# Kernel optimization log

Hardware: AMD Instinct MI355X
Metric: run time of the kernel (lower is better)

## Reference

```python
import jax, jax.numpy as jnp
import numpy as np

B, D, C, Q = 4096, 128, 1000, 65536
PROTO_M = 0.99
EPS = 1e-12


def _l2norm(x, axis=-1):
    n = jnp.sqrt(jnp.sum(x * x, axis=axis, keepdims=True))
    return x / jnp.maximum(n, EPS)


def setup_inputs() -> dict:
    key = jax.random.key(0)
    ks = jax.random.split(key, 7)
    q = _l2norm(jax.random.normal(ks[0], (B, D), dtype=jnp.float32))
    k = _l2norm(jax.random.normal(ks[1], (B, D), dtype=jnp.float32))
    classfy_logits = jax.random.normal(ks[2], (B, C), dtype=jnp.float32)
    plabel = jax.random.uniform(ks[3], (B, C), dtype=jnp.float32)
    prototypes = _l2norm(jax.random.normal(ks[4], (C, D), dtype=jnp.float32))
    queue = _l2norm(jax.random.normal(ks[5], (Q, D), dtype=jnp.float32))
    queue_pseudo = jax.random.randint(ks[6], (Q,), 0, C).astype(jnp.float32)
    return {
        "q": q, "k": k, "classfy_logits": classfy_logits, "plabel": plabel,
        "prototypes": prototypes, "queue": queue, "queue_pseudo": queue_pseudo,
        "ptr": 0,
    }


def reference(q, k, classfy_logits, plabel, prototypes, queue, queue_pseudo, ptr):
    m = PROTO_M
    # classifier softmax (encoder head output)
    classfy_out = jax.nn.softmax(classfy_logits, axis=1)          # [B, C]
    # cluster logits against OLD prototypes (mm happens before EMA update)
    logits_prot = jnp.matmul(q, prototypes.T)                     # [B, C]
    cluster_out = jax.nn.softmax(logits_prot, axis=1)
    # pseudo labels from partial-label-masked scores
    pseudo_labels = jnp.argmax(classfy_out * plabel, axis=1)      # [B] int
    # --- vectorized order-dependent scatter-EMA prototype update ---
    # sequential: proto[l_i] = m*proto[l_i] + (1-m)*q_i  for i = 0..B-1
    # closed form: proto[c]*m^{n_c} + sum_i (1-m)*m^{(#later samples with same label)} q_i
    onehot = (pseudo_labels[:, None] == jnp.arange(C)[None, :])   # [B, C] bool
    counts = jnp.sum(onehot, axis=0)                              # [C] n_c
    rank = jnp.take_along_axis(jnp.cumsum(onehot.astype(jnp.int32), axis=0),
                               pseudo_labels[:, None], axis=1)[:, 0] - 1  # [B]
    n_l = counts[pseudo_labels]                                   # [B]
    w = (1.0 - m) * jnp.power(jnp.float32(m), (n_l - 1 - rank).astype(jnp.float32))
    scatter = jnp.zeros_like(prototypes).at[pseudo_labels].add(w[:, None] * q)
    decay = jnp.power(jnp.float32(m), counts.astype(jnp.float32))[:, None]
    new_prototypes = _l2norm(prototypes * decay + scatter, axis=1)
    # --- MoCo queue enqueue/dequeue (contrastive bank uses OLD queue) ---
    cont_features = jnp.concatenate([q, k, queue], axis=0)        # [2B+Q, D]
    pl_f = pseudo_labels.astype(jnp.float32)
    cont_labels = jnp.concatenate([pl_f, pl_f, queue_pseudo], axis=0)
    new_queue = jax.lax.dynamic_update_slice(queue, k, (ptr, 0))
    new_queue_pseudo = jax.lax.dynamic_update_slice(queue_pseudo, pl_f, (ptr,))
    new_ptr = (ptr + q.shape[0]) % queue.shape[0]
    return (classfy_out, cluster_out, cont_features, cont_labels,
            new_prototypes, new_queue, new_queue_pseudo, new_ptr)
```

## Files before the change

### kernel.cpp

```cpp
#include <hip/hip_runtime.h>
#include <hip/hip_bf16.h>
#include <math.h>

#define Bn 4096
#define Dn 128
#define Cn 1000
#define Qn 65536
#define CPAD 1024

typedef __attribute__((ext_vector_type(8))) short short8v;
typedef __attribute__((ext_vector_type(4))) short short4v;
typedef __attribute__((ext_vector_type(4))) float f32x4;
typedef __attribute__((ext_vector_type(4))) float f4v;

__device__ inline float waveAllMaxF(float v) {
    for (int o = 32; o; o >>= 1) v = fmaxf(v, __shfl_xor(v, o));
    return v;
}
__device__ inline float waveAllSumF(float v) {
    for (int o = 32; o; o >>= 1) v += __shfl_xor(v, o);
    return v;
}
__device__ inline float waveSumF(float v) {
    for (int o = 32; o; o >>= 1) v += __shfl_down(v, o);
    return v;
}
__device__ inline short f2bf(float x) {
    union { __hip_bfloat16 h; short s; } u;
    u.h = __float2bfloat16(x);
    return u.s;
}

__global__ __launch_bounds__(256) void k_phase1(
    const float* __restrict__ logits, const float* __restrict__ plabel,
    const float* __restrict__ q, const float* __restrict__ proto,
    const float* __restrict__ kk, const float* __restrict__ queue,
    const int* __restrict__ ptrp,
    float* __restrict__ out_cls, int* __restrict__ labels,
    __hip_bfloat16* __restrict__ qb, __hip_bfloat16* __restrict__ pb,
    float* __restrict__ out_feat, float* __restrict__ out_queue)
{
    int bid = blockIdx.x, t = threadIdx.x;
    int g = bid / 3, s = bid % 3;

    if (s != 0) {
        int cidx = g * 2 + (s - 1);
        int p = *ptrp;
        int pc = p < 0 ? 0 : (p > Qn - Bn ? Qn - Bn : p);
        const long long QD = (long long)Bn * Dn;
        const long long n4 = (2 * QD + (long long)Qn * Dn) / 4;
        const long long stride = 2048LL * 256;
        for (long long i = (long long)cidx * 256 + t; i < n4; i += stride) {
            long long off = i * 4;
            if (off < QD) {
                *(f4v*)(out_feat + off) = *(const f4v*)(q + off);
            } else if (off < 2 * QD) {
                *(f4v*)(out_feat + off) = *(const f4v*)(kk + off - QD);
            } else {
                long long qoff = off - 2 * QD;
                f4v v = *(const f4v*)(queue + qoff);
                *(f4v*)(out_feat + off) = v;
                int row = (int)(qoff >> 7);
                int col = (int)(qoff & 127);
                unsigned rr = (unsigned)(row - pc);
                if (rr < (unsigned)Bn) v = *(const f4v*)(kk + (long long)rr * Dn + col);
                *(f4v*)(out_queue + qoff) = v;
            }
        }
        return;
    }

    if (t < 160) {
        int idx4 = g * 160 + t;
        if (idx4 < 131072) {
            f4v v = *(const f4v*)(q + (long long)idx4 * 4);
            short4v o = {f2bf(v.x), f2bf(v.y), f2bf(v.z), f2bf(v.w)};
            *(short4v*)((short*)qb + (long long)idx4 * 4) = o;
        } else {
            int j4 = idx4 - 131072;
            short4v o = {0, 0, 0, 0};
            if (j4 < 32000) {
                f4v v = *(const f4v*)(proto + (long long)j4 * 4);
                o = (short4v){f2bf(v.x), f2bf(v.y), f2bf(v.z), f2bf(v.w)};
            }
            *(short4v*)((short*)pb + (long long)j4 * 4) = o;
        }
    }

    int lane = t & 63, wid = t >> 6;
    int row = g * 4 + wid;
    const float* x = logits + (long long)row * Cn;

    float vv[16];
    float mx = -INFINITY;
#pragma unroll
    for (int j = 0; j < 4; ++j) {
        int f4i = lane + j * 64;
        f4v v = (f4v){-INFINITY, -INFINITY, -INFINITY, -INFINITY};
        if (f4i < 250) v = *(const f4v*)(x + f4i * 4);
        vv[j * 4 + 0] = v.x; vv[j * 4 + 1] = v.y;
        vv[j * 4 + 2] = v.z; vv[j * 4 + 3] = v.w;
        mx = fmaxf(mx, fmaxf(fmaxf(v.x, v.y), fmaxf(v.z, v.w)));
    }
    mx = waveAllMaxF(mx);

    float ssum = 0.f;
#pragma unroll
    for (int u = 0; u < 16; ++u) {
        vv[u] = expf(vv[u] - mx);
        ssum += vv[u];
    }
    ssum = waveAllSumF(ssum);
    float inv = 1.f / ssum;

    float bv = -INFINITY; int bi = Cn;
#pragma unroll
    for (int j = 0; j < 4; ++j) {
        int f4i = lane + j * 64;
        if (f4i < 250) {
            float o0 = vv[j * 4 + 0] * inv, o1 = vv[j * 4 + 1] * inv;
            float o2 = vv[j * 4 + 2] * inv, o3 = vv[j * 4 + 3] * inv;
            *((f4v*)(out_cls + (long long)row * Cn) + f4i) = (f4v){o0, o1, o2, o3};
            f4v p4 = *((const f4v*)(plabel + (long long)row * Cn) + f4i);
            float pr[4] = {o0 * p4.x, o1 * p4.y, o2 * p4.z, o3 * p4.w};
#pragma unroll
            for (int jj = 0; jj < 4; ++jj) {
                if (pr[jj] > bv) { bv = pr[jj]; bi = f4i * 4 + jj; }
            }
        }
    }
    for (int o = 32; o; o >>= 1) {
        float ov = __shfl_xor(bv, o);
        int   oi = __shfl_xor(bi, o);
        if (ov > bv || (ov == bv && oi < bi)) { bv = ov; bi = oi; }
    }
    if (lane == 0) labels[row] = bi;
}

__global__ __launch_bounds__(256) void k_phase2(
    const __hip_bfloat16* __restrict__ qb, const __hip_bfloat16* __restrict__ pb,
    const float* __restrict__ proto, const float* __restrict__ q,
    const int* __restrict__ lbl, const float* __restrict__ qps,
    const int* __restrict__ ptrp,
    float* __restrict__ outC, float* __restrict__ outp,
    float* __restrict__ out_lab, float* __restrict__ out_qps,
    float* __restrict__ out_ptr)
{
    __shared__ __align__(16) char smem[32800];
    int bid = blockIdx.x, t = threadIdx.x;

    if (bid < 256) {
        float (*red)[4] = (float (*)[4])smem;
        int lane = t & 63, w = t >> 6;
        int la = lane & 15, lk = lane >> 4;
        int row0 = bid * 16;

        f32x4 acc[16];
#pragma unroll
        for (int j = 0; j < 16; ++j) acc[j] = (f32x4){0.f, 0.f, 0.f, 0.f};

        const short* A = (const short*)qb + (long long)(row0 + la) * Dn;
        const short* Bp = (const short*)pb;
#pragma unroll
        for (int kc = 0; kc < Dn; kc += 32) {
            short8v a = *(const short8v*)(A + kc + lk * 8);
#pragma unroll
            for (int j = 0; j < 16; ++j) {
                int prow = w * 256 + j * 16 + la;
                short8v b = *(const short8v*)(Bp + (long long)prow * Dn + kc + lk * 8);
                acc[j] = __builtin_amdgcn_mfma_f32_16x16x32_bf16(a, b, acc[j], 0, 0, 0);
            }
        }

        float m[4];
#pragma unroll
        for (int rg = 0; rg < 4; ++rg) {
            float v = -INFINITY;
#pragma unroll
            for (int j = 0; j < 16; ++j) {
                int col = w * 256 + j * 16 + la;
                if (col < Cn) v = fmaxf(v, acc[j][rg]);
            }
#pragma unroll
            for (int o = 1; o < 16; o <<= 1) v = fmaxf(v, __shfl_xor(v, o));
            m[rg] = v;
        }
        if (la == 0) {
#pragma unroll
            for (int rg = 0; rg < 4; ++rg) red[lk * 4 + rg][w] = m[rg];
        }
        __syncthreads();
#pragma unroll
        for (int rg = 0; rg < 4; ++rg) {
            int r = lk * 4 + rg;
            m[rg] = fmaxf(fmaxf(red[r][0], red[r][1]), fmaxf(red[r][2], red[r][3]));
        }
        __syncthreads();

        float s[4];
#pragma unroll
        for (int rg = 0; rg < 4; ++rg) {
            float v = 0.f;
#pragma unroll
            for (int j = 0; j < 16; ++j) {
                int col = w * 256 + j * 16 + la;
                float e = (col < Cn) ? expf(acc[j][rg] - m[rg]) : 0.f;
                acc[j][rg] = e;
                v += e;
            }
#pragma unroll
            for (int o = 1; o < 16; o <<= 1) v += __shfl_xor(v, o);
            s[rg] = v;
        }
        if (la == 0) {
#pragma unroll
            for (int rg = 0; rg < 4; ++rg) red[lk * 4 + rg][w] = s[rg];
        }
        __syncthreads();
#pragma unroll
        for (int rg = 0; rg < 4; ++rg) {
            int r = lk * 4 + rg;
            s[rg] = 1.f / (red[r][0] + red[r][1] + red[r][2] + red[r][3]);
        }

#pragma unroll
        for (int j = 0; j < 16; ++j) {
            int col = w * 256 + j * 16 + la;
            if (col < Cn) {
                int rowb = row0 + lk * 4;
#pragma unroll
                for (int rg = 0; rg < 4; ++rg)
                    outC[(long long)(rowb + rg) * Cn + col] = acc[j][rg] * s[rg];
            }
        }
    } else if (bid < 756) {
        int* sl = (int*)smem;
        unsigned short* list0 = (unsigned short*)(smem + 16384);
        unsigned short* list1 = list0 + 4096;
        int* nm = (int*)(smem + 32768);
        float* shh = (float*)(smem + 32776);

        int h = t >> 7, tt = t & 127;
        int c = (bid - 256) * 2 + h;

#pragma unroll
        for (int u = 0; u < 4; ++u) {
            int base = (u * 256 + t) * 4;
            *(int4*)(sl + base) = *(const int4*)(lbl + base);
        }
        if (t == 0)   nm[0] = 0;
        if (t == 128) nm[1] = 0;
        __syncthreads();

        int wv = t >> 6;
        if ((wv & 1) == 0) {
            int hh = wv >> 1;
            int ln = t & 63;
            int cc = (bid - 256) * 2 + hh;
            unsigned short* lst = hh ? list1 : list0;
            int n = 0;
            for (int jj = 0; jj < Bn / 64; ++jj) {
                unsigned long long mask = __ballot(sl[jj * 64 + ln] == cc);
                if (ln == 0) {
                    while (mask) {
                        int b = __builtin_ctzll(mask);
                        lst[n++] = (unsigned short)(jj * 64 + b);
                        mask &= mask - 1;
                    }
                }
            }
            if (ln == 0) nm[hh] = n;
        }
        __syncthreads();

        int n = nm[h];
        unsigned short* lst = h ? list1 : list0;
        float acc = proto[(long long)c * Dn + tt];
        for (int mi = 0; mi < n; ++mi)
            acc = 0.99f * acc + 0.01f * q[(long long)lst[mi] * Dn + tt];

        float ss = waveSumF(acc * acc);
        if ((t & 63) == 0) shh[t >> 6] = ss;
        __syncthreads();
        float nn = sqrtf(shh[h * 2] + shh[h * 2 + 1]);
        outp[(long long)c * Dn + tt] = acc / fmaxf(nn, 1e-12f);
    } else {
        int gid = (bid - 756) * 256 + t;
        const int NL = 2 * Bn + Qn;
        int p = *ptrp;
        int pc = p < 0 ? 0 : (p > Qn - Bn ? Qn - Bn : p);
        if (gid < NL) {
            float v;
            if (gid < Bn)          v = (float)lbl[gid];
            else if (gid < 2 * Bn) v = (float)lbl[gid - Bn];
            else                   v = qps[gid - 2 * Bn];
            out_lab[gid] = v;
        }
        int j = gid - NL;
        if (j >= 0 && j < Qn) {
            unsigned rr = (unsigned)(j - pc);
            out_qps[j] = (rr < (unsigned)Bn) ? (float)lbl[rr] : qps[j];
        }
        if (gid == NL + Qn) out_ptr[0] = (float)((p + Bn) % Qn);
    }
}

extern "C" void kernel_launch(void* const* d_in, const int* in_sizes, int n_in,
                              void* d_out, int out_size, void* d_ws, size_t ws_size,
                              hipStream_t stream)
{
    const float* q     = (const float*)d_in[0];
    const float* kk    = (const float*)d_in[1];
    const float* cl    = (const float*)d_in[2];
    const float* plab  = (const float*)d_in[3];
    const float* proto = (const float*)d_in[4];
    const float* queue = (const float*)d_in[5];
    const float* qps   = (const float*)d_in[6];
    const int*   ptrp  = (const int*)d_in[7];

    float* out = (float*)d_out;
    const long long O_CLU  = 4096000;
    const long long O_FEAT = 8192000;
    const long long O_LAB  = 17629184;
    const long long O_PROT = 17702912;
    const long long O_QUE  = 17830912;
    const long long O_QPS  = 26219520;
    const long long O_PTR  = 26285056;

    char* ws = (char*)d_ws;
    int*   lbl = (int*)(ws + 0);
    __hip_bfloat16* qb = (__hip_bfloat16*)(ws + 1048576);
    __hip_bfloat16* pb = (__hip_bfloat16*)(ws + 2097152);

    k_phase1<<<3072, 256, 0, stream>>>(cl, plab, q, proto, kk, queue, ptrp,
                                       out, lbl, qb, pb, out + O_FEAT, out + O_QUE);
    k_phase2<<<1301, 256, 0, stream>>>(qb, pb, proto, q, lbl, qps, ptrp,
                                       out + O_CLU, out + O_PROT,
                                       out + O_LAB, out + O_QPS, out + O_PTR);
}
```

Before: 49.23 us.

## Split label scan across waves and use closed-form EMA weights for prototype update

The prototype-update blocks no longer stage all labels in shared memory. Each of two waves per class now scans half the label array straight from global memory and builds its own match list. The sequential EMA recurrence is replaced by the closed-form weighted sum with power-based weights, which removes the serial dependency chain so loads can be unrolled and overlapped. Shared memory shrinks, which may allow higher occupancy, but __powf adds approximation error compared with repeated multiplication.

After: 57.16 us. 1.16x slower.

```diff
diff --git a/kernel.cpp b/kernel.cpp
--- a/kernel.cpp
+++ b/kernel.cpp
@@ -146,7 +146,7 @@
     float* __restrict__ out_lab, float* __restrict__ out_qps,
     float* __restrict__ out_ptr)
 {
-    __shared__ __align__(16) char smem[32800];
+    __shared__ __align__(16) char smem[16448];
     int bid = blockIdx.x, t = threadIdx.x;
 
     if (bid < 256) {
@@ -234,56 +234,52 @@
             }
         }
     } else if (bid < 756) {
-        int* sl = (int*)smem;
-        unsigned short* list0 = (unsigned short*)(smem + 16384);
-        unsigned short* list1 = list0 + 4096;
-        int* nm = (int*)(smem + 32768);
-        float* shh = (float*)(smem + 32776);
+        unsigned short* lst = (unsigned short*)smem;
+        int*   nm2 = (int*)(smem + 16384);
+        float* shh = (float*)(smem + 16400);
 
         int h = t >> 7, tt = t & 127;
+        int ln = t & 63, hw = (t >> 6) & 1;
         int c = (bid - 256) * 2 + h;
-
-#pragma unroll
-        for (int u = 0; u < 4; ++u) {
-            int base = (u * 256 + t) * 4;
-            *(int4*)(sl + base) = *(const int4*)(lbl + base);
-        }
-        if (t == 0)   nm[0] = 0;
-        if (t == 128) nm[1] = 0;
-        __syncthreads();
-
-        int wv = t >> 6;
-        if ((wv & 1) == 0) {
-            int hh = wv >> 1;
-            int ln = t & 63;
-            int cc = (bid - 256) * 2 + hh;
-            unsigned short* lst = hh ? list1 : list0;
-            int n = 0;
-            for (int jj = 0; jj < Bn / 64; ++jj) {
-                unsigned long long mask = __ballot(sl[jj * 64 + ln] == cc);
-                if (ln == 0) {
-                    while (mask) {
-                        int b = __builtin_ctzll(mask);
-                        lst[n++] = (unsigned short)(jj * 64 + b);
-                        mask &= mask - 1;
-                    }
+        unsigned short* myl = lst + (h * 2 + hw) * 2048;
+
+        int base = hw * 2048;
+        int n = 0;
+        for (int jj = 0; jj < 32; ++jj) {
+            int lj = lbl[base + jj * 64 + ln];
+            unsigned long long mask = __ballot(lj == c);
+            if (ln == 0) {
+                while (mask) {
+                    int b = __builtin_ctzll(mask);
+                    myl[n++] = (unsigned short)(base + jj * 64 + b);
+                    mask &= mask - 1;
                 }
             }
-            if (ln == 0) nm[hh] = n;
-        }
-        __syncthreads();
-
-        int n = nm[h];
-        unsigned short* lst = h ? list1 : list0;
-        float acc = proto[(long long)c * Dn + tt];
-        for (int mi = 0; mi < n; ++mi)
-            acc = 0.99f * acc + 0.01f * q[(long long)lst[mi] * Dn + tt];
-
-        float ss = waveSumF(acc * acc);
-        if ((t & 63) == 0) shh[t >> 6] = ss;
-        __syncthreads();
-        float nn = sqrtf(shh[h * 2] + shh[h * 2 + 1]);
-        outp[(long long)c * Dn + tt] = acc / fmaxf(nn, 1e-12f);
+        }
+        if (ln == 0) nm2[h * 2 + hw] = n;
+        __syncthreads();
+
+        int n0 = nm2[h * 2 + 0];
+        int n1 = nm2[h * 2 + 1];
+        int nn = n0 + n1;
+        const unsigned short* l0 = lst + (h * 2 + 0) * 2048;
+        const unsigned short* l1 = lst + (h * 2 + 1) * 2048;
+
+        float acc = 0.f;
+#pragma unroll 4
+        for (int mi = 0; mi < nn; ++mi) {
+            int r = (mi < n0) ? l0[mi] : l1[mi - n0];
+            float wv = 0.01f * __powf(0.99f, (float)(nn - 1 - mi));
+            acc += wv * q[(long long)r * Dn + tt];
+        }
+        float decay = __powf(0.99f, (float)nn);
+        float v = proto[(long long)c * Dn + tt] * decay + acc;
+
+        float ss = waveSumF(v * v);
+        if (ln == 0) shh[t >> 6] = ss;
+        __syncthreads();
+        float nrm = sqrtf(shh[h * 2] + shh[h * 2 + 1]);
+        outp[(long long)c * Dn + tt] = v / fmaxf(nrm, 1e-12f);
     } else {
         int gid = (bid - 756) * 256 + t;
         const int NL = 2 * Bn + Qn;
```
